# Performance work log

Hardware: AMD Instinct MI355X
Metric: run time of the kernel (lower is better)

The kernel has to match this reference:

```python
import jax, jax.numpy as jnp
import numpy as np
from functools import partial

OBS, LATENT, HID = 32, 256, 1024


def setup_inputs() -> dict:
    key = jax.random.key(0)
    ks = jax.random.split(key, 16)
    s = 0.05  # small init keeps tanh/relu activations in a healthy range
    B, T = 128, 256
    inp = {
        "y": jax.random.normal(ks[0], (B, T, OBS), dtype=jnp.float32),
        "horizon": 512,
        # tanh-RNN cell params (torch nn.RNN layout: W_ih [H,I], W_hh [H,H])
        "W_ih": jax.random.normal(ks[1], (LATENT, OBS), dtype=jnp.float32) * s,
        "W_hh": jax.random.normal(ks[2], (LATENT, LATENT), dtype=jnp.float32) * s,
        "b_ih": jax.random.normal(ks[3], (LATENT,), dtype=jnp.float32) * s,
        "b_hh": jax.random.normal(ks[4], (LATENT,), dtype=jnp.float32) * s,
        # psi: 5-layer MLP latent -> hid -> hid -> hid -> hid -> obs
        "W1": jax.random.normal(ks[5], (HID, LATENT), dtype=jnp.float32) * s,
        "b1": jnp.zeros((HID,), dtype=jnp.float32),
        "W2": jax.random.normal(ks[6], (HID, HID), dtype=jnp.float32) * s,
        "b2": jnp.zeros((HID,), dtype=jnp.float32),
        "W3": jax.random.normal(ks[7], (HID, HID), dtype=jnp.float32) * s,
        "b3": jnp.zeros((HID,), dtype=jnp.float32),
        "W4": jax.random.normal(ks[8], (HID, HID), dtype=jnp.float32) * s,
        "b4": jnp.zeros((HID,), dtype=jnp.float32),
        "W5": jax.random.normal(ks[9], (OBS, HID), dtype=jnp.float32) * s,
        "b5": jnp.zeros((OBS,), dtype=jnp.float32),
    }
    return inp


def _psi(z, W1, b1, W2, b2, W3, b3, W4, b4, W5, b5):
    h = jax.nn.relu(z @ W1.T + b1)
    h = jax.nn.relu(h @ W2.T + b2)
    h = jax.nn.relu(h @ W3.T + b3)
    h = jax.nn.relu(h @ W4.T + b4)
    return h @ W5.T + b5  # (B, OBS)


def reference(y, horizon, W_ih, W_hh, b_ih, b_hh,
              W1, b1, W2, b2, W3, b3, W4, b4, W5, b5):
    B, T, S = y.shape
    psi = partial(_psi, W1=W1, b1=b1, W2=W2, b2=b2, W3=W3, b3=b3,
                  W4=W4, b4=b4, W5=W5, b5=b5)

    def cell(z, inp):
        return jnp.tanh(inp @ W_ih.T + b_ih + z @ W_hh.T + b_hh)

    z0 = jnp.zeros((B, y.shape[2]), dtype=y.dtype) if False else jnp.zeros((B, W_hh.shape[0]), dtype=y.dtype)

    # Phase 1: teacher-forced. y_hat[t] = psi(z_t) BEFORE consuming y[:, t].
    def step_tf(z, y_t):
        yh = psi(z)
        return cell(z, y_t), yh

    z, yh1 = jax.lax.scan(step_tf, z0, jnp.swapaxes(y, 0, 1))  # yh1: (T,B,S)

    def step_ar(z, _):
        yh = psi(z)
        return cell(z, yh), yh

    z, yh2 = jax.lax.scan(step_ar, z, None, length=horizon - T)  # (H-T,B,S)

    y_hat = jnp.concatenate([yh1, yh2], axis=0)  # (H,B,S)
    return jnp.swapaxes(y_hat, 0, 1)  # (B,H,S)
```

## Files before the change

### kernel.cpp

```cpp
#include <hip/hip_runtime.h>
#include <stdint.h>


#define BATCH 128
#define TTF   256
#define HOR   512
#define OBS   32
#define LAT   256
#define HID   1024

#define GROUPS  8
#define MEMBERS 32
#define ARBLOCKS (GROUPS * MEMBERS)
#define ARTHREADS 128

typedef __attribute__((ext_vector_type(8))) short short8;
typedef __attribute__((ext_vector_type(4))) float floatx4;

#define OFF_WB1   ((size_t)0)
#define OFF_WB2   (OFF_WB1 + (size_t)HID*LAT*2)
#define OFF_WB3   (OFF_WB2 + (size_t)HID*HID*2)
#define OFF_WB4   (OFF_WB3 + (size_t)HID*HID*2)
#define OFF_WB5   (OFF_WB4 + (size_t)HID*HID*2)
#define OFF_CB    (OFF_WB5 + (size_t)OBS*HID*2)
#define OFF_WHH2  (OFF_CB + (size_t)LAT*4)
#define OFF_WIH2  (OFF_WHH2 + (size_t)64*256*8)
#define OFF_ZF    (OFF_WIH2 + (size_t)8*256*8)
#define OFF_Z     (OFF_ZF + (size_t)BATCH*LAT*4)
#define OFF_WBC   (OFF_Z + (size_t)BATCH*TTF*LAT*2)
#define OFF_HB    (OFF_WBC + (size_t)LAT*288*2)
#define OFF_CTR   (OFF_HB + (size_t)GROUPS*8*16*HID*2)
#define OFF_END   (OFF_CTR + (size_t)GROUPS*512)

__device__ __forceinline__ uint16_t f2bf(float f) {
    uint32_t u = __float_as_uint(f);
    u += 0x7fffu + ((u >> 16) & 1u);
    return (uint16_t)(u >> 16);
}
__device__ __forceinline__ float bflo(uint32_t u) { return __uint_as_float(u << 16); }
__device__ __forceinline__ float bfhi(uint32_t u) { return __uint_as_float(u & 0xffff0000u); }

__device__ __forceinline__ float fast_tanh(float x) {
    float ax = fabsf(x);
    float e  = __expf(-2.f * ax);
    float r  = (1.f - e) / (1.f + e);
    return copysignf(r, x);
}

__device__ __forceinline__ int hswz(int row, int col) {
    return row * 1024 + ((((col >> 3) ^ (row & 7)) << 3) | (col & 7));
}
__device__ __forceinline__ int zswz(int row, int col) {
    return row * 256 + ((((col >> 3) ^ (row & 7)) << 3) | (col & 7));
}

__device__ __forceinline__ void st16_mall(void* p, floatx4 v) {
    asm volatile("global_store_dwordx4 %0, %1, off sc0 sc1"
                 :: "v"(p), "v"(v) : "memory");
}

typedef const __attribute__((address_space(1))) void* gas_t;
typedef __attribute__((address_space(3))) void* las_t;
__device__ __forceinline__ void gl_lds16(const void* g, void* l) {
    __builtin_amdgcn_global_load_lds((gas_t)g, (las_t)l, 16, 0, 0x11);
}

__device__ __forceinline__ void stage_h(const uint16_t* src, uint16_t* dst,
                                        int w, int L) {
    const char* gp = (const char*)src + w * 16384 + L * 16;
    char* lp = (char*)dst + w * 16384;
    #pragma unroll
    for (int i = 0; i < 16; i++)
        gl_lds16(gp + i * 1024, lp + i * 1024);
}

__global__ void k_cvt(const float* __restrict__ s, uint16_t* __restrict__ d, int n) {
    int i = blockIdx.x * 256 + threadIdx.x;
    if (i < n) d[i] = f2bf(s[i]);
}

__global__ void k_cb(const float* __restrict__ a, const float* __restrict__ b,
                     float* __restrict__ c) {
    int j = threadIdx.x;
    c[j] = a[j] + b[j];
}

__global__ void k_pack(const float* __restrict__ w, uint2* __restrict__ dst, int klen) {
    int k4 = blockIdx.x, j = threadIdx.x;
    int k = k4 * 4;
    uint32_t a = f2bf(w[(size_t)j * klen + k + 0]);
    uint32_t b = f2bf(w[(size_t)j * klen + k + 1]);
    uint32_t c = f2bf(w[(size_t)j * klen + k + 2]);
    uint32_t d = f2bf(w[(size_t)j * klen + k + 3]);
    uint2 r; r.x = a | (b << 16); r.y = c | (d << 16);
    dst[k4 * 256 + j] = r;
}

__global__ void k_packc(const float* __restrict__ whh, const float* __restrict__ wih,
                        uint16_t* __restrict__ wbc) {
    int col = blockIdx.x;
    for (int k = threadIdx.x; k < 288; k += 256) {
        float v = (k < 256) ? whh[(size_t)col * 256 + k] : wih[(size_t)col * 32 + (k - 256)];
        wbc[(size_t)col * 288 + k] = f2bf(v);
    }
}

__global__ __launch_bounds__(256) void k_rnn_tf(
    const float* __restrict__ y, const uint2* __restrict__ whh2,
    const uint2* __restrict__ wih2, const float* __restrict__ cb,
    uint16_t* __restrict__ Zg, float* __restrict__ zfinal)
{
    __shared__ alignas(16) float zl[LAT];
    __shared__ alignas(16) float ys[OBS];
    int j = threadIdx.x, b = blockIdx.x;
    zl[j] = 0.f;
    __syncthreads();
    const float4* z4 = (const float4*)zl;
    const float4* y4 = (const float4*)ys;
    for (int t = 0; t < TTF; t++) {
        if (j < OBS) ys[j] = y[(size_t)b * (TTF * OBS) + t * OBS + j];
        Zg[((size_t)b * TTF + t) * LAT + j] = f2bf(zl[j]);
        __syncthreads();
        float acc = cb[j];
        #pragma unroll 8
        for (int k4 = 0; k4 < 64; k4++) {
            uint2 wv = whh2[k4 * 256 + j];
            float4 zq = z4[k4];
            acc += bflo(wv.x) * zq.x + bfhi(wv.x) * zq.y
                 + bflo(wv.y) * zq.z + bfhi(wv.y) * zq.w;
        }
        #pragma unroll
        for (int k4 = 0; k4 < 8; k4++) {
            uint2 wv = wih2[k4 * 256 + j];
            float4 yq = y4[k4];
            acc += bflo(wv.x) * yq.x + bfhi(wv.x) * yq.y
                 + bflo(wv.y) * yq.z + bfhi(wv.y) * yq.w;
        }
        __syncthreads();
        zl[j] = fast_tanh(acc);
    }
    __syncthreads();
    zfinal[(size_t)b * LAT + j] = zl[j];
}

__global__ __launch_bounds__(512) void k_psi_bulk(
    const uint16_t* __restrict__ Zg,
    const uint16_t* __restrict__ wb1, const uint16_t* __restrict__ wb2,
    const uint16_t* __restrict__ wb3, const uint16_t* __restrict__ wb4,
    const uint16_t* __restrict__ wb5,
    const float* __restrict__ b1, const float* __restrict__ b2,
    const float* __restrict__ b3, const float* __restrict__ b4,
    const float* __restrict__ b5, float* __restrict__ out)
{
    __shared__ uint16_t hbuf[32 * 1024];
    int tid = threadIdx.x;
    int w = tid >> 6, L = tid & 63, lm = L & 15, q = L >> 4;
    int rb = blockIdx.x * 32;
    int colbase = w * 128;
    floatx4 acc[2][8];
    const floatx4 zero = {0.f, 0.f, 0.f, 0.f};

    #pragma unroll
    for (int mt = 0; mt < 2; mt++)
        #pragma unroll
        for (int nt = 0; nt < 8; nt++) acc[mt][nt] = zero;
    for (int kc = 0; kc < 8; kc++) {
        short8 a0 = *(const short8*)(Zg + (size_t)(rb + lm) * LAT + kc * 32 + q * 8);
        short8 a1 = *(const short8*)(Zg + (size_t)(rb + 16 + lm) * LAT + kc * 32 + q * 8);
        #pragma unroll
        for (int nt = 0; nt < 8; nt++) {
            int n = colbase + nt * 16 + lm;
            short8 bf = *(const short8*)(wb1 + (size_t)n * LAT + kc * 32 + q * 8);
            acc[0][nt] = __builtin_amdgcn_mfma_f32_16x16x32_bf16(a0, bf, acc[0][nt], 0, 0, 0);
            acc[1][nt] = __builtin_amdgcn_mfma_f32_16x16x32_bf16(a1, bf, acc[1][nt], 0, 0, 0);
        }
    }
    #pragma unroll
    for (int mt = 0; mt < 2; mt++)
        #pragma unroll
        for (int nt = 0; nt < 8; nt++) {
            int col = colbase + nt * 16 + lm;
            float bias = b1[col];
            #pragma unroll
            for (int i = 0; i < 4; i++) {
                int row = mt * 16 + q * 4 + i;
                hbuf[hswz(row, col)] = f2bf(fmaxf(acc[mt][nt][i] + bias, 0.f));
            }
        }
    __syncthreads();

    const uint16_t* wbs[3] = {wb2, wb3, wb4};
    const float*    bbs[3] = {b2, b3, b4};
    for (int ll = 0; ll < 3; ll++) {
        const uint16_t* wb = wbs[ll];
        const float* bb = bbs[ll];
        #pragma unroll
        for (int mt = 0; mt < 2; mt++)
            #pragma unroll
            for (int nt = 0; nt < 8; nt++) acc[mt][nt] = zero;
        for (int kc = 0; kc < 32; kc++) {
            int g = ((kc * 4 + q) ^ (lm & 7)) << 3;
            short8 a0 = *(const short8*)(hbuf + lm * 1024 + g);
            short8 a1 = *(const short8*)(hbuf + (16 + lm) * 1024 + g);
            #pragma unroll
            for (int nt = 0; nt < 8; nt++) {
                int n = colbase + nt * 16 + lm;
                short8 bf = *(const short8*)(wb + (size_t)n * HID + kc * 32 + q * 8);
                acc[0][nt] = __builtin_amdgcn_mfma_f32_16x16x32_bf16(a0, bf, acc[0][nt], 0, 0, 0);
                acc[1][nt] = __builtin_amdgcn_mfma_f32_16x16x32_bf16(a1, bf, acc[1][nt], 0, 0, 0);
            }
        }
        __syncthreads();
        #pragma unroll
        for (int mt = 0; mt < 2; mt++)
            #pragma unroll
            for (int nt = 0; nt < 8; nt++) {
                int col = colbase + nt * 16 + lm;
                float bias = bb[col];
                #pragma unroll
                for (int i = 0; i < 4; i++) {
                    int row = mt * 16 + q * 4 + i;
                    hbuf[hswz(row, col)] = f2bf(fmaxf(acc[mt][nt][i] + bias, 0.f));
                }
            }
        __syncthreads();
    }

    if (w < 4) {
        int mt = w >> 1;
        int nb = (w & 1) * 16;
        floatx4 a5 = zero;
        for (int kc = 0; kc < 32; kc++) {
            int g = ((kc * 4 + q) ^ (lm & 7)) << 3;
            short8 a = *(const short8*)(hbuf + (mt * 16 + lm) * 1024 + g);
            short8 bf = *(const short8*)(wb5 + (size_t)(nb + lm) * HID + kc * 32 + q * 8);
            a5 = __builtin_amdgcn_mfma_f32_16x16x32_bf16(a, bf, a5, 0, 0, 0);
        }
        int col = nb + lm;
        float bias = b5[col];
        #pragma unroll
        for (int i = 0; i < 4; i++) {
            int row = mt * 16 + q * 4 + i;
            int r = rb + row;
            int bb_ = r >> 8, tt = r & 255;
            out[(size_t)bb_ * (HOR * OBS) + tt * OBS + col] = a5[i] + bias;
        }
    }
}

__global__ __launch_bounds__(ARTHREADS) void k_ar2(
    const float* __restrict__ zfinal,
    const uint16_t* __restrict__ wb1, const uint16_t* __restrict__ wb2,
    const uint16_t* __restrict__ wb3, const uint16_t* __restrict__ wb4,
    const uint16_t* __restrict__ wb5, const uint16_t* __restrict__ wbc,
    const float* __restrict__ b1g, const float* __restrict__ b2g,
    const float* __restrict__ b3g, const float* __restrict__ b4g,
    const float* __restrict__ b5g, const float* __restrict__ cb,
    uint16_t* __restrict__ hb_all, unsigned* __restrict__ ctr_all,
    float* __restrict__ out)
{
    __shared__ alignas(16) uint16_t hstg[16 * 1024];
    __shared__ alignas(16) uint16_t zst[2 * 16 * 256];
    __shared__ alignas(16) uint16_t yscr[16 * 32];
    __shared__ alignas(16) uint16_t hsl[16 * 32];

    const int tid = threadIdx.x;
    const int g = blockIdx.x >> 5, m = blockIdx.x & 31;
    const int w = tid >> 6, L = tid & 63, lm = L & 15, q = L >> 4, lm7 = lm & 7;
    const int colbase = m * 32;
    const int cl = w * 16 + lm;
    const int rb = g * 16;
    uint16_t* hb = hb_all + (size_t)g * (8 * 16 * HID);
    unsigned* ctr = ctr_all + g * 128;
    const floatx4 zero = {0.f, 0.f, 0.f, 0.f};

    const float b1v = b1g[colbase + cl];
    const float b2v = b2g[colbase + cl];
    const float b3v = b3g[colbase + cl];
    const float b4v = b4g[colbase + cl];
    const float b5v = b5g[cl];
    float cbv[8];
    #pragma unroll
    for (int ct = 0; ct < 8; ct++) cbv[ct] = cb[w * 128 + ct * 16 + lm];

    for (int idx = tid; idx < 16 * 256; idx += ARTHREADS) {
        int r = idx >> 8, c = idx & 255;
        zst[zswz(r, c)] = f2bf(zfinal[(size_t)(rb + r) * LAT + c]);
    }
    __syncthreads();

    #define HOP_ARRIVE(DST) do {                                             \
        __syncthreads();                                                     \
        if (tid < 64) {                                                      \
            int row_ = tid >> 2, gr_ = tid & 3;                              \
            floatx4 vv_ = *(const floatx4*)((const char*)hsl + tid * 16);    \
            int gsw_ = (m * 4 + gr_) ^ (row_ & 7);                           \
            st16_mall((char*)(DST) + row_ * 2048 + gsw_ * 16, vv_);          \
            asm volatile("s_waitcnt vmcnt(0)" ::: "memory");                 \
            if (tid == 0)                                                    \
                __hip_atomic_fetch_add(ctr, 1u, __ATOMIC_RELAXED,            \
                                       __HIP_MEMORY_SCOPE_AGENT);            \
        }                                                                    \
    } while (0)

    #define HOP_WAIT(TGT) do {                                               \
        if (tid == 0) {                                                      \
            while (__hip_atomic_load(ctr, __ATOMIC_RELAXED,                  \
                                     __HIP_MEMORY_SCOPE_AGENT) < (TGT)) {}   \
        }                                                                    \
        __syncthreads();                                                     \
    } while (0)

    #define CCZ(K0, K1) do {                                                 \
        _Pragma("unroll")                                                    \
        for (int ct = 0; ct < 8; ct++) {                                     \
            const uint16_t* bb2_ = wbc + (size_t)(w * 128 + ct * 16 + lm) * 288 + q * 8; \
            _Pragma("unroll")                                                \
            for (int kc = (K0); kc < (K1); kc++) {                           \
                int gz_ = (kc * 4 + q) ^ lm7;                                \
                short8 a_ = *(const short8*)(zcur + lm * 256 + gz_ * 8);     \
                short8 b_ = *(const short8*)(bb2_ + kc * 32);                \
                cc[ct] = __builtin_amdgcn_mfma_f32_16x16x32_bf16(a_, b_, cc[ct], 0, 0, 0); \
            }                                                                \
        }                                                                    \
    } while (0)

    #define MID_COMPUTE(WB, BV) do {                                         \
        floatx4 acc_ = zero;                                                 \
        const uint16_t* bb_ = WB + (size_t)(colbase + cl) * HID + q * 8;     \
        _Pragma("unroll 8")                                                  \
        for (int kc = 0; kc < 32; kc++) {                                    \
            int gh = (kc * 4 + q) ^ lm7;                                     \
            short8 a_ = *(const short8*)(hstg + lm * 1024 + gh * 8);         \
            short8 b_ = *(const short8*)(bb_ + kc * 32);                     \
            acc_ = __builtin_amdgcn_mfma_f32_16x16x32_bf16(a_, b_, acc_, 0, 0, 0); \
        }                                                                    \
        _Pragma("unroll")                                                    \
        for (int i = 0; i < 4; i++)                                          \
            hsl[(q * 4 + i) * 32 + cl] = f2bf(fmaxf(acc_[i] + (BV), 0.f));   \
    } while (0)

    unsigned tgt = 0;
    #pragma unroll 1
    for (int t = 0; t < HOR - TTF; t++) {
        uint16_t* zcur = zst + (t & 1) * (16 * 256);
        uint16_t* znx  = zst + ((t + 1) & 1) * (16 * 256);
        uint16_t* hp = hb + (t & 1) * (4 * 16 * HID);
        uint16_t* h1 = hp;
        uint16_t* h2 = hp + 16 * HID;
        uint16_t* h3 = hp + 2 * 16 * HID;
        uint16_t* h4 = hp + 3 * 16 * HID;

        floatx4 cc[8];
        #pragma unroll
        for (int ct = 0; ct < 8; ct++) cc[ct] = zero;

        {
            floatx4 acc = zero;
            const uint16_t* bb = wb1 + (size_t)(colbase + cl) * LAT + q * 8;
            #pragma unroll
            for (int kc = 0; kc < 8; kc++) {
                int gz = (kc * 4 + q) ^ lm7;
                short8 a = *(const short8*)(zcur + lm * 256 + gz * 8);
                short8 b = *(const short8*)(bb + kc * 32);
                acc = __builtin_amdgcn_mfma_f32_16x16x32_bf16(a, b, acc, 0, 0, 0);
            }
            #pragma unroll
            for (int i = 0; i < 4; i++)
                hsl[(q * 4 + i) * 32 + cl] = f2bf(fmaxf(acc[i] + b1v, 0.f));
        }
        HOP_ARRIVE(h1); tgt += MEMBERS;
        CCZ(0, 2);
        HOP_WAIT(tgt);
        stage_h(h1, hstg, w, L);
        __syncthreads();

        MID_COMPUTE(wb2, b2v);
        HOP_ARRIVE(h2); tgt += MEMBERS;
        CCZ(2, 4);
        HOP_WAIT(tgt);
        stage_h(h2, hstg, w, L);
        __syncthreads();

        MID_COMPUTE(wb3, b3v);
        HOP_ARRIVE(h3); tgt += MEMBERS;
        CCZ(4, 6);
        HOP_WAIT(tgt);
        stage_h(h3, hstg, w, L);
        __syncthreads();

        MID_COMPUTE(wb4, b4v);
        HOP_ARRIVE(h4); tgt += MEMBERS;
        CCZ(6, 8);
        HOP_WAIT(tgt);
        stage_h(h4, hstg, w, L);
        __syncthreads();

        {
            floatx4 a5 = zero;
            const uint16_t* bb = wb5 + (size_t)cl * HID + q * 8;
            #pragma unroll 8
            for (int kc = 0; kc < 32; kc++) {
                int gh = (kc * 4 + q) ^ lm7;
                short8 a = *(const short8*)(hstg + lm * 1024 + gh * 8);
                short8 b = *(const short8*)(bb + kc * 32);
                a5 = __builtin_amdgcn_mfma_f32_16x16x32_bf16(a, b, a5, 0, 0, 0);
            }
            float vout[4];
            #pragma unroll
            for (int i = 0; i < 4; i++) {
                float v = a5[i] + b5v;
                vout[i] = v;
                yscr[(q * 4 + i) * 32 + cl] = f2bf(v);
            }
            if (m == 0) {
                #pragma unroll
                for (int i = 0; i < 4; i++)
                    out[(size_t)(rb + q * 4 + i) * (HOR * OBS) + (TTF + t) * OBS + cl] = vout[i];
            }
        }
        __syncthreads();
        {
            short8 ay = *(const short8*)(yscr + lm * 32 + q * 8);
            #pragma unroll
            for (int ct = 0; ct < 8; ct++) {
                int ccol = w * 128 + ct * 16 + lm;
                const uint16_t* bb2 = wbc + (size_t)ccol * 288 + q * 8;
                short8 b = *(const short8*)(bb2 + 8 * 32);
                floatx4 v = __builtin_amdgcn_mfma_f32_16x16x32_bf16(ay, b, cc[ct], 0, 0, 0);
                #pragma unroll
                for (int i = 0; i < 4; i++)
                    znx[zswz(q * 4 + i, ccol)] = f2bf(fast_tanh(v[i] + cbv[ct]));
            }
        }
        __syncthreads();
    }
    #undef MID_COMPUTE
    #undef CCZ
    #undef HOP_WAIT
    #undef HOP_ARRIVE
}

extern "C" void kernel_launch(void* const* d_in, const int* in_sizes, int n_in,
                              void* d_out, int out_size, void* d_ws, size_t ws_size,
                              hipStream_t stream) {
    (void)in_sizes; (void)n_in; (void)out_size; (void)ws_size;
    const float* y    = (const float*)d_in[0];
    const float* W_ih = (const float*)d_in[2];
    const float* W_hh = (const float*)d_in[3];
    const float* b_ih = (const float*)d_in[4];
    const float* b_hh = (const float*)d_in[5];
    const float* W1   = (const float*)d_in[6];
    const float* b1   = (const float*)d_in[7];
    const float* W2   = (const float*)d_in[8];
    const float* b2   = (const float*)d_in[9];
    const float* W3   = (const float*)d_in[10];
    const float* b3   = (const float*)d_in[11];
    const float* W4   = (const float*)d_in[12];
    const float* b4   = (const float*)d_in[13];
    const float* W5   = (const float*)d_in[14];
    const float* b5   = (const float*)d_in[15];
    float* out = (float*)d_out;
    char* ws = (char*)d_ws;

    uint16_t* WB1  = (uint16_t*)(ws + OFF_WB1);
    uint16_t* WB2  = (uint16_t*)(ws + OFF_WB2);
    uint16_t* WB3  = (uint16_t*)(ws + OFF_WB3);
    uint16_t* WB4  = (uint16_t*)(ws + OFF_WB4);
    uint16_t* WB5  = (uint16_t*)(ws + OFF_WB5);
    float*    CB   = (float*)(ws + OFF_CB);
    uint2*    WHH2 = (uint2*)(ws + OFF_WHH2);
    uint2*    WIH2 = (uint2*)(ws + OFF_WIH2);
    float*    ZF   = (float*)(ws + OFF_ZF);
    uint16_t* Zbuf = (uint16_t*)(ws + OFF_Z);
    uint16_t* WBC  = (uint16_t*)(ws + OFF_WBC);
    uint16_t* HB   = (uint16_t*)(ws + OFF_HB);
    unsigned* CTR  = (unsigned*)(ws + OFF_CTR);

    k_cvt<<<(HID*LAT + 255) / 256, 256, 0, stream>>>(W1, WB1, HID * LAT);
    k_cvt<<<(HID*HID + 255) / 256, 256, 0, stream>>>(W2, WB2, HID * HID);
    k_cvt<<<(HID*HID + 255) / 256, 256, 0, stream>>>(W3, WB3, HID * HID);
    k_cvt<<<(HID*HID + 255) / 256, 256, 0, stream>>>(W4, WB4, HID * HID);
    k_cvt<<<(OBS*HID + 255) / 256, 256, 0, stream>>>(W5, WB5, OBS * HID);
    k_cb<<<1, 256, 0, stream>>>(b_ih, b_hh, CB);
    k_pack<<<64, 256, 0, stream>>>(W_hh, WHH2, LAT);
    k_pack<<<8, 256, 0, stream>>>(W_ih, WIH2, OBS);
    k_packc<<<256, 256, 0, stream>>>(W_hh, W_ih, WBC);
    hipMemsetAsync(CTR, 0, GROUPS * 512, stream);

    k_rnn_tf<<<BATCH, 256, 0, stream>>>(y, WHH2, WIH2, CB, Zbuf, ZF);

    k_psi_bulk<<<(BATCH * TTF) / 32, 512, 0, stream>>>(
        Zbuf, WB1, WB2, WB3, WB4, WB5, b1, b2, b3, b4, b5, out);

    void* args[] = {
        (void*)&ZF, (void*)&WB1, (void*)&WB2, (void*)&WB3, (void*)&WB4,
        (void*)&WB5, (void*)&WBC, (void*)&b1, (void*)&b2, (void*)&b3,
        (void*)&b4, (void*)&b5, (void*)&CB, (void*)&HB, (void*)&CTR,
        (void*)&out
    };
    hipError_t ce = hipLaunchCooperativeKernel((const void*)k_ar2,
                                               dim3(ARBLOCKS), dim3(ARTHREADS),
                                               args, 0, stream);
    if (ce != hipSuccess) {
        (void)hipGetLastError();
        k_ar2<<<dim3(ARBLOCKS), dim3(ARTHREADS), 0, stream>>>(
            ZF, WB1, WB2, WB3, WB4, WB5, WBC, b1, b2, b3, b4, b5, CB,
            HB, CTR, out);
    }
}
```

Before: 6.633 ms.

## Compute final psi layer as split-K partials reduced via global atomics

Instead of publishing the fourth hidden layer to global memory and having every block stage all 1024 columns and run the full layer-5 matmul, each member block now computes a partial layer-5 product from its own 32 hidden columns. It atomically adds that partial into a per-group double-buffered float accumulator, which is zeroed one step ahead. After the group barrier, each block loads only the 16x32 reduced result. This removes the 32 KB stage of h4 and the 32-step MFMA loop per block, in exchange for float atomics, an extra block-level sync, and a summation order that is no longer deterministic.

Result: slower. 8.587 ms (+29.4%).

```diff
diff --git a/kernel.cpp b/kernel.cpp
--- a/kernel.cpp
+++ b/kernel.cpp
@@ -30,7 +30,8 @@
 #define OFF_WBC   (OFF_Z + (size_t)BATCH*TTF*LAT*2)
 #define OFF_HB    (OFF_WBC + (size_t)LAT*288*2)
 #define OFF_CTR   (OFF_HB + (size_t)GROUPS*8*16*HID*2)
-#define OFF_END   (OFF_CTR + (size_t)GROUPS*512)
+#define OFF_YH    (OFF_CTR + (size_t)GROUPS*512)
+#define OFF_END   (OFF_YH + (size_t)GROUPS*4096)
 
 __device__ __forceinline__ uint16_t f2bf(float f) {
     uint32_t u = __float_as_uint(f);
@@ -257,12 +258,13 @@
     const float* __restrict__ b3g, const float* __restrict__ b4g,
     const float* __restrict__ b5g, const float* __restrict__ cb,
     uint16_t* __restrict__ hb_all, unsigned* __restrict__ ctr_all,
-    float* __restrict__ out)
+    float* __restrict__ yh_all, float* __restrict__ out)
 {
     __shared__ alignas(16) uint16_t hstg[16 * 1024];
     __shared__ alignas(16) uint16_t zst[2 * 16 * 256];
     __shared__ alignas(16) uint16_t yscr[16 * 32];
     __shared__ alignas(16) uint16_t hsl[16 * 32];
+    __shared__ alignas(16) float yhf[512];
 
     const int tid = threadIdx.x;
     const int g = blockIdx.x >> 5, m = blockIdx.x & 31;
@@ -272,6 +274,7 @@
     const int rb = g * 16;
     uint16_t* hb = hb_all + (size_t)g * (8 * 16 * HID);
     unsigned* ctr = ctr_all + g * 128;
+    float* yhg = yh_all + g * 1024;
     const floatx4 zero = {0.f, 0.f, 0.f, 0.f};
 
     const float b1v = b1g[colbase + cl];
@@ -349,7 +352,8 @@
         uint16_t* h1 = hp;
         uint16_t* h2 = hp + 16 * HID;
         uint16_t* h3 = hp + 2 * 16 * HID;
-        uint16_t* h4 = hp + 3 * 16 * HID;
+        float* ya  = yhg + (t & 1) * 512;
+        float* yaz = yhg + ((t + 1) & 1) * 512;
 
         floatx4 cc[8];
         #pragma unroll
@@ -372,6 +376,10 @@
         HOP_ARRIVE(h1); tgt += MEMBERS;
         CCZ(0, 2);
         HOP_WAIT(tgt);
+        if (tid < 64) {
+            st16_mall((char*)yaz + tid * 32, zero);
+            st16_mall((char*)yaz + tid * 32 + 16, zero);
+        }
         stage_h(h1, hstg, w, L);
         __syncthreads();
 
@@ -390,26 +398,31 @@
         __syncthreads();
 
         MID_COMPUTE(wb4, b4v);
-        HOP_ARRIVE(h4); tgt += MEMBERS;
+        __syncthreads();
+        {
+            short8 a = *(const short8*)(hsl + lm * 32 + q * 8);
+            short8 b = *(const short8*)(wb5 + (size_t)(w * 16 + lm) * HID + m * 32 + q * 8);
+            floatx4 p = __builtin_amdgcn_mfma_f32_16x16x32_bf16(a, b, zero, 0, 0, 0);
+            #pragma unroll
+            for (int i = 0; i < 4; i++)
+                __hip_atomic_fetch_add(ya + (q * 4 + i) * 32 + w * 16 + lm, p[i],
+                                       __ATOMIC_RELAXED, __HIP_MEMORY_SCOPE_AGENT);
+            asm volatile("s_waitcnt vmcnt(0)" ::: "memory");
+        }
+        __syncthreads();
+        if (tid == 0)
+            __hip_atomic_fetch_add(ctr, 1u, __ATOMIC_RELAXED, __HIP_MEMORY_SCOPE_AGENT);
+        tgt += MEMBERS;
         CCZ(6, 8);
         HOP_WAIT(tgt);
-        stage_h(h4, hstg, w, L);
+        gl_lds16((const char*)ya + w * 1024 + L * 16, (char*)yhf + w * 1024 + L * 16);
         __syncthreads();
 
         {
-            floatx4 a5 = zero;
-            const uint16_t* bb = wb5 + (size_t)cl * HID + q * 8;
-            #pragma unroll 8
-            for (int kc = 0; kc < 32; kc++) {
-                int gh = (kc * 4 + q) ^ lm7;
-                short8 a = *(const short8*)(hstg + lm * 1024 + gh * 8);
-                short8 b = *(const short8*)(bb + kc * 32);
-                a5 = __builtin_amdgcn_mfma_f32_16x16x32_bf16(a, b, a5, 0, 0, 0);
-            }
             float vout[4];
             #pragma unroll
             for (int i = 0; i < 4; i++) {
-                float v = a5[i] + b5v;
+                float v = yhf[(q * 4 + i) * 32 + cl] + b5v;
                 vout[i] = v;
                 yscr[(q * 4 + i) * 32 + cl] = f2bf(v);
             }
@@ -476,6 +489,7 @@
     uint16_t* WBC  = (uint16_t*)(ws + OFF_WBC);
     uint16_t* HB   = (uint16_t*)(ws + OFF_HB);
     unsigned* CTR  = (unsigned*)(ws + OFF_CTR);
+    float*    YH   = (float*)(ws + OFF_YH);
 
     k_cvt<<<(HID*LAT + 255) / 256, 256, 0, stream>>>(W1, WB1, HID * LAT);
     k_cvt<<<(HID*HID + 255) / 256, 256, 0, stream>>>(W2, WB2, HID * HID);
@@ -486,7 +500,7 @@
     k_pack<<<64, 256, 0, stream>>>(W_hh, WHH2, LAT);
     k_pack<<<8, 256, 0, stream>>>(W_ih, WIH2, OBS);
     k_packc<<<256, 256, 0, stream>>>(W_hh, W_ih, WBC);
-    hipMemsetAsync(CTR, 0, GROUPS * 512, stream);
+    hipMemsetAsync(CTR, 0, GROUPS * 512 + GROUPS * 4096, stream);
 
     k_rnn_tf<<<BATCH, 256, 0, stream>>>(y, WHH2, WIH2, CB, Zbuf, ZF);
 
@@ -497,7 +511,7 @@
         (void*)&ZF, (void*)&WB1, (void*)&WB2, (void*)&WB3, (void*)&WB4,
         (void*)&WB5, (void*)&WBC, (void*)&b1, (void*)&b2, (void*)&b3,
         (void*)&b4, (void*)&b5, (void*)&CB, (void*)&HB, (void*)&CTR,
-        (void*)&out
+        (void*)&YH, (void*)&out
     };
     hipError_t ce = hipLaunchCooperativeKernel((const void*)k_ar2,
                                                dim3(ARBLOCKS), dim3(ARTHREADS),
@@ -506,6 +520,6 @@
         (void)hipGetLastError();
         k_ar2<<<dim3(ARBLOCKS), dim3(ARTHREADS), 0, stream>>>(
             ZF, WB1, WB2, WB3, WB4, WB5, WBC, b1, b2, b3, b4, b5, CB,
-            HB, CTR, out);
-    }
-}
+            HB, CTR, YH, out);
+    }
+}
```

## Split fused psi MLP into per-layer GEMM kernels over row chunks

Applied to the files above, without the earlier changes.

Replaces the single fused k_psi_bulk kernel (one block per 32 rows running all five layers out of shared memory) with separate per-layer MFMA GEMM kernels, processed in chunks of 8192 rows and staged through two bf16 global scratch buffers. Each layer now launches 8x more blocks, splitting the columns so more CUs work at once. The cost is extra global-memory traffic for the intermediate activations and more kernel launches. The new path only runs when the workspace is large enough, otherwise the fused kernel is kept.

After: 7.925 ms. 1.19x slower.

```diff
diff --git a/kernel.cpp b/kernel.cpp
--- a/kernel.cpp
+++ b/kernel.cpp
@@ -13,6 +13,8 @@
 #define MEMBERS 32
 #define ARBLOCKS (GROUPS * MEMBERS)
 #define ARTHREADS 128
+
+#define PSI_CHUNK 8192
 
 typedef __attribute__((ext_vector_type(8))) short short8;
 typedef __attribute__((ext_vector_type(4))) float floatx4;
@@ -30,7 +32,9 @@
 #define OFF_WBC   (OFF_Z + (size_t)BATCH*TTF*LAT*2)
 #define OFF_HB    (OFF_WBC + (size_t)LAT*288*2)
 #define OFF_CTR   (OFF_HB + (size_t)GROUPS*8*16*HID*2)
-#define OFF_END   (OFF_CTR + (size_t)GROUPS*512)
+#define OFF_HA    (OFF_CTR + (size_t)GROUPS*512)
+#define OFF_HBF   (OFF_HA + (size_t)PSI_CHUNK*HID*2)
+#define OFF_END   (OFF_HBF + (size_t)PSI_CHUNK*HID*2)
 
 __device__ __forceinline__ uint16_t f2bf(float f) {
     uint32_t u = __float_as_uint(f);
@@ -141,6 +145,102 @@
     }
     __syncthreads();
     zfinal[(size_t)b * LAT + j] = zl[j];
+}
+
+__global__ __launch_bounds__(512) void k_psi_l1(
+    const uint16_t* __restrict__ zin,
+    const uint16_t* __restrict__ wb,
+    const float* __restrict__ bias, uint16_t* __restrict__ hout)
+{
+    const int tid = threadIdx.x;
+    const int w = tid >> 6, L = tid & 63, lm = L & 15, q = L >> 4;
+    const int c = blockIdx.x & 7, rt = blockIdx.x >> 3;
+    const int rb = rt * 32;
+    const int rf = w & 1, cp = w >> 1;
+    const int cbase = c * 128 + cp * 32;
+    floatx4 acc0 = {0.f,0.f,0.f,0.f}, acc1 = {0.f,0.f,0.f,0.f};
+    const uint16_t* ap  = zin + (size_t)(rb + rf * 16 + lm) * LAT + q * 8;
+    const uint16_t* bp0 = wb + (size_t)(cbase + lm) * LAT + q * 8;
+    const uint16_t* bp1 = wb + (size_t)(cbase + 16 + lm) * LAT + q * 8;
+    #pragma unroll
+    for (int kc = 0; kc < 8; kc++) {
+        short8 a  = *(const short8*)(ap  + kc * 32);
+        short8 b0 = *(const short8*)(bp0 + kc * 32);
+        short8 b1 = *(const short8*)(bp1 + kc * 32);
+        acc0 = __builtin_amdgcn_mfma_f32_16x16x32_bf16(a, b0, acc0, 0, 0, 0);
+        acc1 = __builtin_amdgcn_mfma_f32_16x16x32_bf16(a, b1, acc1, 0, 0, 0);
+    }
+    float bv0 = bias[cbase + lm], bv1 = bias[cbase + 16 + lm];
+    #pragma unroll
+    for (int i = 0; i < 4; i++) {
+        int row = rb + rf * 16 + q * 4 + i;
+        hout[(size_t)row * HID + cbase + lm]      = f2bf(fmaxf(acc0[i] + bv0, 0.f));
+        hout[(size_t)row * HID + cbase + 16 + lm] = f2bf(fmaxf(acc1[i] + bv1, 0.f));
+    }
+}
+
+__global__ __launch_bounds__(512) void k_psi_mid(
+    const uint16_t* __restrict__ hin,
+    const uint16_t* __restrict__ wb,
+    const float* __restrict__ bias, uint16_t* __restrict__ hout)
+{
+    const int tid = threadIdx.x;
+    const int w = tid >> 6, L = tid & 63, lm = L & 15, q = L >> 4;
+    const int c = blockIdx.x & 7, rt = blockIdx.x >> 3;
+    const int rb = rt * 32;
+    const int rf = w & 1, cp = w >> 1;
+    const int cbase = c * 128 + cp * 32;
+    floatx4 acc0 = {0.f,0.f,0.f,0.f}, acc1 = {0.f,0.f,0.f,0.f};
+    const uint16_t* ap  = hin + (size_t)(rb + rf * 16 + lm) * HID + q * 8;
+    const uint16_t* bp0 = wb + (size_t)(cbase + lm) * HID + q * 8;
+    const uint16_t* bp1 = wb + (size_t)(cbase + 16 + lm) * HID + q * 8;
+    #pragma unroll 8
+    for (int kc = 0; kc < 32; kc++) {
+        short8 a  = *(const short8*)(ap  + kc * 32);
+        short8 b0 = *(const short8*)(bp0 + kc * 32);
+        short8 b1 = *(const short8*)(bp1 + kc * 32);
+        acc0 = __builtin_amdgcn_mfma_f32_16x16x32_bf16(a, b0, acc0, 0, 0, 0);
+        acc1 = __builtin_amdgcn_mfma_f32_16x16x32_bf16(a, b1, acc1, 0, 0, 0);
+    }
+    float bv0 = bias[cbase + lm], bv1 = bias[cbase + 16 + lm];
+    #pragma unroll
+    for (int i = 0; i < 4; i++) {
+        int row = rb + rf * 16 + q * 4 + i;
+        hout[(size_t)row * HID + cbase + lm]      = f2bf(fmaxf(acc0[i] + bv0, 0.f));
+        hout[(size_t)row * HID + cbase + 16 + lm] = f2bf(fmaxf(acc1[i] + bv1, 0.f));
+    }
+}
+
+__global__ __launch_bounds__(128) void k_psi_l5(
+    const uint16_t* __restrict__ hin,
+    const uint16_t* __restrict__ wb5,
+    const float* __restrict__ bias, float* __restrict__ out, int row0)
+{
+    const int tid = threadIdx.x;
+    const int w = tid >> 6, L = tid & 63, lm = L & 15, q = L >> 4;
+    const int rt = blockIdx.x;
+    const int rb = rt * 32;
+    const int rf = w;
+    floatx4 acc0 = {0.f,0.f,0.f,0.f}, acc1 = {0.f,0.f,0.f,0.f};
+    const uint16_t* ap  = hin + (size_t)(rb + rf * 16 + lm) * HID + q * 8;
+    const uint16_t* bp0 = wb5 + (size_t)lm * HID + q * 8;
+    const uint16_t* bp1 = wb5 + (size_t)(16 + lm) * HID + q * 8;
+    #pragma unroll 8
+    for (int kc = 0; kc < 32; kc++) {
+        short8 a  = *(const short8*)(ap  + kc * 32);
+        short8 b0 = *(const short8*)(bp0 + kc * 32);
+        short8 b1 = *(const short8*)(bp1 + kc * 32);
+        acc0 = __builtin_amdgcn_mfma_f32_16x16x32_bf16(a, b0, acc0, 0, 0, 0);
+        acc1 = __builtin_amdgcn_mfma_f32_16x16x32_bf16(a, b1, acc1, 0, 0, 0);
+    }
+    float bv0 = bias[lm], bv1 = bias[16 + lm];
+    #pragma unroll
+    for (int i = 0; i < 4; i++) {
+        int gr = row0 + rb + rf * 16 + q * 4 + i;
+        int bb = gr >> 8, tt = gr & 255;
+        out[(size_t)bb * (HOR * OBS) + tt * OBS + lm]      = acc0[i] + bv0;
+        out[(size_t)bb * (HOR * OBS) + tt * OBS + 16 + lm] = acc1[i] + bv1;
+    }
 }
 
 __global__ __launch_bounds__(512) void k_psi_bulk(
@@ -444,7 +544,7 @@
 extern "C" void kernel_launch(void* const* d_in, const int* in_sizes, int n_in,
                               void* d_out, int out_size, void* d_ws, size_t ws_size,
                               hipStream_t stream) {
-    (void)in_sizes; (void)n_in; (void)out_size; (void)ws_size;
+    (void)in_sizes; (void)n_in; (void)out_size;
     const float* y    = (const float*)d_in[0];
     const float* W_ih = (const float*)d_in[2];
     const float* W_hh = (const float*)d_in[3];
@@ -476,6 +576,8 @@
     uint16_t* WBC  = (uint16_t*)(ws + OFF_WBC);
     uint16_t* HB   = (uint16_t*)(ws + OFF_HB);
     unsigned* CTR  = (unsigned*)(ws + OFF_CTR);
+    uint16_t* HA   = (uint16_t*)(ws + OFF_HA);
+    uint16_t* HBF  = (uint16_t*)(ws + OFF_HBF);
 
     k_cvt<<<(HID*LAT + 255) / 256, 256, 0, stream>>>(W1, WB1, HID * LAT);
     k_cvt<<<(HID*HID + 255) / 256, 256, 0, stream>>>(W2, WB2, HID * HID);
@@ -490,8 +592,21 @@
 
     k_rnn_tf<<<BATCH, 256, 0, stream>>>(y, WHH2, WIH2, CB, Zbuf, ZF);
 
-    k_psi_bulk<<<(BATCH * TTF) / 32, 512, 0, stream>>>(
-        Zbuf, WB1, WB2, WB3, WB4, WB5, b1, b2, b3, b4, b5, out);
+    if (ws_size >= OFF_END) {
+        const int NCHUNK = (BATCH * TTF) / PSI_CHUNK;
+        for (int ch = 0; ch < NCHUNK; ch++) {
+            const uint16_t* zin = Zbuf + (size_t)ch * PSI_CHUNK * LAT;
+            k_psi_l1 <<<(PSI_CHUNK/32)*8, 512, 0, stream>>>(zin, WB1, b1, HA);
+            k_psi_mid<<<(PSI_CHUNK/32)*8, 512, 0, stream>>>(HA, WB2, b2, HBF);
+            k_psi_mid<<<(PSI_CHUNK/32)*8, 512, 0, stream>>>(HBF, WB3, b3, HA);
+            k_psi_mid<<<(PSI_CHUNK/32)*8, 512, 0, stream>>>(HA, WB4, b4, HBF);
+            k_psi_l5 <<<PSI_CHUNK/32, 128, 0, stream>>>(HBF, WB5, b5, out,
+                                                        ch * PSI_CHUNK);
+        }
+    } else {
+        k_psi_bulk<<<(BATCH * TTF) / 32, 512, 0, stream>>>(
+            Zbuf, WB1, WB2, WB3, WB4, WB5, b1, b2, b3, b4, b5, out);
+    }
 
     void* args[] = {
         (void*)&ZF, (void*)&WB1, (void*)&WB2, (void*)&WB3, (void*)&WB4,
```
